# Performance work log

Hardware: AMD Instinct MI355X
Metric: run time of the kernel (lower is better)

The kernel has to match this reference:

```python
import jax, jax.numpy as jnp
import numpy as np

B, L, F = 16, 2048, 512


def setup_inputs() -> dict:
    key = jax.random.key(0)
    k1, k2 = jax.random.split(key)
    feature = jax.random.normal(k1, (B, L, F), dtype=jnp.float32)
    noise = jax.random.normal(k2, (B, L, L), dtype=jnp.float32)
    return {"feature": feature, "noise": noise}


def reference(feature, noise):
    # augmenting_path = softmax over last dim of (B, L, L) gaussian noise
    augmenting_path = jax.nn.softmax(noise, axis=-1)
    # einsum 'bij,bjf->bif': mix frames along the sequence dim
    augmented_feature = jnp.einsum('bij,bjf->bif', augmenting_path, feature)
    return augmented_feature
```

## Files before the change

kernel.cpp:

```cpp
#include <hip/hip_runtime.h>
#include <hip/hip_bf16.h>


#define NB 16
#define SL 2048
#define NF 512
#define TM 128
#define BK 32
#define NT 512
#define NKB (SL / BK)

typedef __bf16 bf16x8 __attribute__((ext_vector_type(8)));
typedef float  f32x4  __attribute__((ext_vector_type(4)));

__device__ __forceinline__ unsigned int f2bf(float x) {
    union { float f; unsigned int u; } v; v.f = x;
    return (v.u + 0x7FFFu + ((v.u >> 16) & 1u)) >> 16;
}

__global__ __launch_bounds__(256, 4)
void feat_panelize(const float* __restrict__ feat, unsigned short* __restrict__ featP) {
    __shared__ unsigned short Lt[32][270];
    const int t  = threadIdx.x;
    const int n0 = blockIdx.x * 256;
    const int kb = blockIdx.y;
    const int b  = blockIdx.z;
    const float* src = feat + ((size_t)b * SL + (size_t)kb * BK) * NF + n0;
    const int j  = t >> 3;
    const int c0 = (t & 7) << 2;
    #pragma unroll
    for (int c = 0; c < 8; ++c) {
        const float4 v = *(const float4*)(src + (size_t)j * NF + c0 + (c << 5));
        unsigned short* p = &Lt[j][c0 + (c << 5)];
        p[0] = (unsigned short)f2bf(v.x); p[1] = (unsigned short)f2bf(v.y);
        p[2] = (unsigned short)f2bf(v.z); p[3] = (unsigned short)f2bf(v.w);
    }
    __syncthreads();
    unsigned int w[16];
    #pragma unroll
    for (int m = 0; m < 16; ++m)
        w[m] = (unsigned int)Lt[2 * m][t] | ((unsigned int)Lt[2 * m + 1][t] << 16);
    unsigned short* dst = featP + ((size_t)(b * NKB + kb) * NF + (size_t)(n0 + t)) * BK;
    #pragma unroll
    for (int c = 0; c < 4; ++c)
        *(uint4*)(dst + (c << 3)) = *(const uint4*)&w[c << 2];
}

__global__ __launch_bounds__(NT, 2)
void frame_augment(const float* __restrict__ noise,
                   const unsigned short* __restrict__ featP,
                   float* __restrict__ out) {
    __shared__ __align__(16) unsigned short As[2][TM][BK];
    __shared__ __align__(16) unsigned short Bs[2][NF][BK];
    __shared__ float part[TM][4];
    __shared__ float linv[TM];

    const int tid  = threadIdx.x;
    const int lane = tid & 63;
    const int wv   = tid >> 6;
    const int n    = blockIdx.x;
    const int b    = ((n & 7) << 1) | ((n >> 3) & 1);
    const int i0   = (n >> 4) * TM;

    const float* noise_b = noise + ((size_t)b * SL + i0) * SL;
    const unsigned short* featB = featP + (size_t)b * NKB * NF * BK;
    float* out_b = out + ((size_t)b * SL + i0) * NF;

    const int ar = tid >> 2;
    const int ac = (tid & 3) << 3;
    const int fm = lane & 15;
    const int fq = lane >> 4;

    f32x4 acc[8][4];
    #pragma unroll
    for (int mi = 0; mi < 8; ++mi)
        #pragma unroll
        for (int ni = 0; ni < 4; ++ni)
            acc[mi][ni] = (f32x4){0.f, 0.f, 0.f, 0.f};

    float rowsum = 0.f;
    const float* a_src = noise_b + (size_t)ar * SL + ac;

    float4 nv0 = *(const float4*)(a_src);
    float4 nv1 = *(const float4*)(a_src + 4);
    {
        const float e0=__expf(nv0.x), e1=__expf(nv0.y), e2=__expf(nv0.z), e3=__expf(nv0.w);
        const float e4=__expf(nv1.x), e5=__expf(nv1.y), e6=__expf(nv1.z), e7=__expf(nv1.w);
        rowsum += ((e0+e1)+(e2+e3)) + ((e4+e5)+(e6+e7));
        uint4 p;
        p.x = f2bf(e0) | (f2bf(e1) << 16);  p.y = f2bf(e2) | (f2bf(e3) << 16);
        p.z = f2bf(e4) | (f2bf(e5) << 16);  p.w = f2bf(e6) | (f2bf(e7) << 16);
        *(uint4*)&As[0][ar][ac] = p;
    }
    {
        const unsigned short* panel = featB;
        #pragma unroll
        for (int c = 0; c < 4; ++c) {
            const int q = (c << 9) + tid;
            __builtin_amdgcn_global_load_lds(
                (const __attribute__((address_space(1))) unsigned int*)(panel + (size_t)q * 8),
                (__attribute__((address_space(3))) unsigned int*)&Bs[0][q >> 2][(q & 3) << 3],
                16, 0, 0);
        }
    }
    nv0 = *(const float4*)(a_src + BK);
    nv1 = *(const float4*)(a_src + BK + 4);
    __syncthreads();

    for (int kb = 0; kb < NKB; ++kb) {
        const int cur = kb & 1, nxt = cur ^ 1;

        if (kb + 1 < NKB) {
            const unsigned short* panel = featB + (size_t)(kb + 1) * NF * BK;
            #pragma unroll
            for (int c = 0; c < 4; ++c) {
                const int q = (c << 9) + tid;
                __builtin_amdgcn_global_load_lds(
                    (const __attribute__((address_space(1))) unsigned int*)(panel + (size_t)q * 8),
                    (__attribute__((address_space(3))) unsigned int*)&Bs[nxt][q >> 2][(q & 3) << 3],
                    16, 0, 0);
            }
            const float e0=__expf(nv0.x), e1=__expf(nv0.y), e2=__expf(nv0.z), e3=__expf(nv0.w);
            const float e4=__expf(nv1.x), e5=__expf(nv1.y), e6=__expf(nv1.z), e7=__expf(nv1.w);
            rowsum += ((e0+e1)+(e2+e3)) + ((e4+e5)+(e6+e7));
            uint4 p;
            p.x = f2bf(e0) | (f2bf(e1) << 16);  p.y = f2bf(e2) | (f2bf(e3) << 16);
            p.z = f2bf(e4) | (f2bf(e5) << 16);  p.w = f2bf(e6) | (f2bf(e7) << 16);
            *(uint4*)&As[nxt][ar][ac] = p;
        }
        if (kb + 2 < NKB) {
            nv0 = *(const float4*)(a_src + (size_t)(kb + 2) * BK);
            nv1 = *(const float4*)(a_src + (size_t)(kb + 2) * BK + 4);
        }

        bf16x8 af[8], bfr[4];
        #pragma unroll
        for (int mi = 0; mi < 8; ++mi)
            af[mi] = *(const bf16x8*)&As[cur][mi * 16 + fm][fq << 3];
        #pragma unroll
        for (int ni = 0; ni < 4; ++ni)
            bfr[ni] = *(const bf16x8*)&Bs[cur][(wv << 6) + ni * 16 + fm][fq << 3];
        #pragma unroll
        for (int mi = 0; mi < 8; ++mi)
            #pragma unroll
            for (int ni = 0; ni < 4; ++ni)
                acc[mi][ni] = __builtin_amdgcn_mfma_f32_16x16x32_bf16(
                    af[mi], bfr[ni], acc[mi][ni], 0, 0, 0);
        __syncthreads();
    }

    part[ar][tid & 3] = rowsum;
    __syncthreads();
    if (tid < TM) {
        const float* q = part[tid];
        linv[tid] = 1.0f / (((q[0] + q[1]) + (q[2] + q[3])));
    }
    __syncthreads();

    #pragma unroll
    for (int mi = 0; mi < 8; ++mi) {
        #pragma unroll
        for (int r = 0; r < 4; ++r) {
            const int row = mi * 16 + (fq << 2) + r;
            const float sc = linv[row];
            float* orow = out_b + (size_t)row * NF + (wv << 6) + fm;
            #pragma unroll
            for (int ni = 0; ni < 4; ++ni)
                orow[ni * 16] = acc[mi][ni][r] * sc;
        }
    }
}

extern "C" void kernel_launch(void* const* d_in, const int* in_sizes, int n_in,
                              void* d_out, int out_size, void* d_ws, size_t ws_size,
                              hipStream_t stream) {
    (void)in_sizes; (void)n_in; (void)out_size; (void)ws_size;
    const float* feat  = (const float*)d_in[0];
    const float* noise = (const float*)d_in[1];
    float* outp = (float*)d_out;
    unsigned short* featP = (unsigned short*)d_ws;

    feat_panelize<<<dim3(NF / 256, NKB, NB), 256, 0, stream>>>(feat, featP);
    frame_augment<<<dim3(SL / TM * NB), NT, 0, stream>>>(noise, featP, outp);
}
```

Before: 461.3 us.

## Read B fragments directly from global, double K tile, pad A in LDS

The feature panel is no longer staged through shared memory. Each wave now loads its B fragments straight from the pre-panelized global buffer into registers. The K tile doubles to 64 and the loop is unrolled by two, which halves the number of barriers, and the exp/softmax staging for the next tile is interleaved between the two MFMA halves. A rows are padded to a stride of 72 to reduce LDS bank conflicts, and removing Bs frees most of the LDS, at the cost of relying on L2/global latency for B with no explicit prefetch.

```diff
diff --git a/kernel.cpp b/kernel.cpp
--- a/kernel.cpp
+++ b/kernel.cpp
@@ -6,9 +6,11 @@
 #define SL 2048
 #define NF 512
 #define TM 128
-#define BK 32
+#define BK 64
+#define NKB (SL / BK)
+#define NPKB (SL / 32)
 #define NT 512
-#define NKB (SL / BK)
+#define ASTRIDE 72
 
 typedef __bf16 bf16x8 __attribute__((ext_vector_type(8)));
 typedef float  f32x4  __attribute__((ext_vector_type(4)));
@@ -25,7 +27,7 @@
     const int n0 = blockIdx.x * 256;
     const int kb = blockIdx.y;
     const int b  = blockIdx.z;
-    const float* src = feat + ((size_t)b * SL + (size_t)kb * BK) * NF + n0;
+    const float* src = feat + ((size_t)b * SL + (size_t)kb * 32) * NF + n0;
     const int j  = t >> 3;
     const int c0 = (t & 7) << 2;
     #pragma unroll
@@ -40,18 +42,71 @@
     #pragma unroll
     for (int m = 0; m < 16; ++m)
         w[m] = (unsigned int)Lt[2 * m][t] | ((unsigned int)Lt[2 * m + 1][t] << 16);
-    unsigned short* dst = featP + ((size_t)(b * NKB + kb) * NF + (size_t)(n0 + t)) * BK;
+    unsigned short* dst = featP + ((size_t)(b * NPKB + kb) * NF + (size_t)(n0 + t)) * 32;
     #pragma unroll
     for (int c = 0; c < 4; ++c)
         *(uint4*)(dst + (c << 3)) = *(const uint4*)&w[c << 2];
 }
+
+
+#define FA_BODY(KB, CUR, CONS, LOADB)                                          \
+    {                                                                          \
+        const int kb_ = (KB);                                                  \
+        const int nxt_ = (CUR) ^ 1;                                            \
+        if (kb_ + 2 < NKB) {                                                   \
+            const float* np_ = a_src + (size_t)(kb_ + 2) * BK;                 \
+            _Pragma("unroll")                                                  \
+            for (int c = 0; c < 4; ++c) LOADB[c] = *(const float4*)(np_ + (c << 2)); \
+        }                                                                      \
+        const unsigned short* pan_ = featB + (size_t)(kb_ << 1) * (NF * 32);   \
+        bf16x8 bfr0[4], bfr1[4];                                               \
+        _Pragma("unroll")                                                      \
+        for (int ni = 0; ni < 4; ++ni)                                         \
+            bfr0[ni] = *(const bf16x8*)(pan_ + (size_t)(((wv << 6) + (ni << 4) + fm) << 5) + (fq << 3)); \
+        _Pragma("unroll")                                                      \
+        for (int ni = 0; ni < 4; ++ni)                                         \
+            bfr1[ni] = *(const bf16x8*)(pan_ + NF * 32 + (size_t)(((wv << 6) + (ni << 4) + fm) << 5) + (fq << 3)); \
+        _Pragma("unroll")                                                      \
+        for (int mi = 0; mi < 8; ++mi) {                                       \
+            const bf16x8 af_ = *(const bf16x8*)&As[CUR][(mi << 4) + fm][fq << 3]; \
+            _Pragma("unroll")                                                  \
+            for (int ni = 0; ni < 4; ++ni)                                     \
+                acc[mi][ni] = __builtin_amdgcn_mfma_f32_16x16x32_bf16(af_, bfr0[ni], acc[mi][ni], 0, 0, 0); \
+        }                                                                      \
+        if (kb_ + 1 < NKB) {                                                   \
+            const float e0_ = __expf(CONS[0].x), e1_ = __expf(CONS[0].y);      \
+            const float e2_ = __expf(CONS[0].z), e3_ = __expf(CONS[0].w);      \
+            const float e4_ = __expf(CONS[1].x), e5_ = __expf(CONS[1].y);      \
+            const float e6_ = __expf(CONS[1].z), e7_ = __expf(CONS[1].w);      \
+            const float e8_ = __expf(CONS[2].x), e9_ = __expf(CONS[2].y);      \
+            const float ea_ = __expf(CONS[2].z), eb_ = __expf(CONS[2].w);      \
+            const float ec_ = __expf(CONS[3].x), ed_ = __expf(CONS[3].y);      \
+            const float ee_ = __expf(CONS[3].z), ef_ = __expf(CONS[3].w);      \
+            rowsum += (((e0_+e1_)+(e2_+e3_)) + ((e4_+e5_)+(e6_+e7_)))          \
+                    + (((e8_+e9_)+(ea_+eb_)) + ((ec_+ed_)+(ee_+ef_)));         \
+            uint4 q0_, q1_;                                                    \
+            q0_.x = f2bf(e0_) | (f2bf(e1_) << 16); q0_.y = f2bf(e2_) | (f2bf(e3_) << 16); \
+            q0_.z = f2bf(e4_) | (f2bf(e5_) << 16); q0_.w = f2bf(e6_) | (f2bf(e7_) << 16); \
+            q1_.x = f2bf(e8_) | (f2bf(e9_) << 16); q1_.y = f2bf(ea_) | (f2bf(eb_) << 16); \
+            q1_.z = f2bf(ec_) | (f2bf(ed_) << 16); q1_.w = f2bf(ee_) | (f2bf(ef_) << 16); \
+            *(uint4*)&As[nxt_][ar][ac] = q0_;                                  \
+            *(uint4*)&As[nxt_][ar][ac + 8] = q1_;                              \
+        }                                                                      \
+        _Pragma("unroll")                                                      \
+        for (int mi = 0; mi < 8; ++mi) {                                       \
+            const bf16x8 af_ = *(const bf16x8*)&As[CUR][(mi << 4) + fm][32 + (fq << 3)]; \
+            _Pragma("unroll")                                                  \
+            for (int ni = 0; ni < 4; ++ni)                                     \
+                acc[mi][ni] = __builtin_amdgcn_mfma_f32_16x16x32_bf16(af_, bfr1[ni], acc[mi][ni], 0, 0, 0); \
+        }                                                                      \
+        __syncthreads();                                                       \
+    }
 
 __global__ __launch_bounds__(NT, 2)
 void frame_augment(const float* __restrict__ noise,
                    const unsigned short* __restrict__ featP,
                    float* __restrict__ out) {
-    __shared__ __align__(16) unsigned short As[2][TM][BK];
-    __shared__ __align__(16) unsigned short Bs[2][NF][BK];
+    __shared__ __align__(16) unsigned short As[2][TM][ASTRIDE];
     __shared__ float part[TM][4];
     __shared__ float linv[TM];
 
@@ -63,11 +118,11 @@
     const int i0   = (n >> 4) * TM;
 
     const float* noise_b = noise + ((size_t)b * SL + i0) * SL;
-    const unsigned short* featB = featP + (size_t)b * NKB * NF * BK;
+    const unsigned short* featB = featP + (size_t)b * NPKB * NF * 32;
     float* out_b = out + ((size_t)b * SL + i0) * NF;
 
     const int ar = tid >> 2;
-    const int ac = (tid & 3) << 3;
+    const int ac = (tid & 3) << 4;
     const int fm = lane & 15;
     const int fq = lane >> 4;
 
@@ -81,79 +136,42 @@
     float rowsum = 0.f;
     const float* a_src = noise_b + (size_t)ar * SL + ac;
 
-    float4 nv0 = *(const float4*)(a_src);
-    float4 nv1 = *(const float4*)(a_src + 4);
+    float4 nvA[4], nvB[4];
+    #pragma unroll
+    for (int c = 0; c < 4; ++c) nvB[c] = *(const float4*)(a_src + (c << 2));
     {
-        const float e0=__expf(nv0.x), e1=__expf(nv0.y), e2=__expf(nv0.z), e3=__expf(nv0.w);
-        const float e4=__expf(nv1.x), e5=__expf(nv1.y), e6=__expf(nv1.z), e7=__expf(nv1.w);
-        rowsum += ((e0+e1)+(e2+e3)) + ((e4+e5)+(e6+e7));
-        uint4 p;
-        p.x = f2bf(e0) | (f2bf(e1) << 16);  p.y = f2bf(e2) | (f2bf(e3) << 16);
-        p.z = f2bf(e4) | (f2bf(e5) << 16);  p.w = f2bf(e6) | (f2bf(e7) << 16);
-        *(uint4*)&As[0][ar][ac] = p;
-    }
-    {
-        const unsigned short* panel = featB;
-        #pragma unroll
-        for (int c = 0; c < 4; ++c) {
-            const int q = (c << 9) + tid;
-            __builtin_amdgcn_global_load_lds(
-                (const __attribute__((address_space(1))) unsigned int*)(panel + (size_t)q * 8),
-                (__attribute__((address_space(3))) unsigned int*)&Bs[0][q >> 2][(q & 3) << 3],
-                16, 0, 0);
-        }
-    }
-    nv0 = *(const float4*)(a_src + BK);
-    nv1 = *(const float4*)(a_src + BK + 4);
-    __syncthreads();
-
-    for (int kb = 0; kb < NKB; ++kb) {
-        const int cur = kb & 1, nxt = cur ^ 1;
-
-        if (kb + 1 < NKB) {
-            const unsigned short* panel = featB + (size_t)(kb + 1) * NF * BK;
-            #pragma unroll
-            for (int c = 0; c < 4; ++c) {
-                const int q = (c << 9) + tid;
-                __builtin_amdgcn_global_load_lds(
-                    (const __attribute__((address_space(1))) unsigned int*)(panel + (size_t)q * 8),
-                    (__attribute__((address_space(3))) unsigned int*)&Bs[nxt][q >> 2][(q & 3) << 3],
-                    16, 0, 0);
-            }
-            const float e0=__expf(nv0.x), e1=__expf(nv0.y), e2=__expf(nv0.z), e3=__expf(nv0.w);
-            const float e4=__expf(nv1.x), e5=__expf(nv1.y), e6=__expf(nv1.z), e7=__expf(nv1.w);
-            rowsum += ((e0+e1)+(e2+e3)) + ((e4+e5)+(e6+e7));
-            uint4 p;
-            p.x = f2bf(e0) | (f2bf(e1) << 16);  p.y = f2bf(e2) | (f2bf(e3) << 16);
-            p.z = f2bf(e4) | (f2bf(e5) << 16);  p.w = f2bf(e6) | (f2bf(e7) << 16);
-            *(uint4*)&As[nxt][ar][ac] = p;
-        }
-        if (kb + 2 < NKB) {
-            nv0 = *(const float4*)(a_src + (size_t)(kb + 2) * BK);
-            nv1 = *(const float4*)(a_src + (size_t)(kb + 2) * BK + 4);
-        }
-
-        bf16x8 af[8], bfr[4];
-        #pragma unroll
-        for (int mi = 0; mi < 8; ++mi)
-            af[mi] = *(const bf16x8*)&As[cur][mi * 16 + fm][fq << 3];
-        #pragma unroll
-        for (int ni = 0; ni < 4; ++ni)
-            bfr[ni] = *(const bf16x8*)&Bs[cur][(wv << 6) + ni * 16 + fm][fq << 3];
-        #pragma unroll
-        for (int mi = 0; mi < 8; ++mi)
-            #pragma unroll
-            for (int ni = 0; ni < 4; ++ni)
-                acc[mi][ni] = __builtin_amdgcn_mfma_f32_16x16x32_bf16(
-                    af[mi], bfr[ni], acc[mi][ni], 0, 0, 0);
-        __syncthreads();
+        const float e0 = __expf(nvB[0].x), e1 = __expf(nvB[0].y);
+        const float e2 = __expf(nvB[0].z), e3 = __expf(nvB[0].w);
+        const float e4 = __expf(nvB[1].x), e5 = __expf(nvB[1].y);
+        const float e6 = __expf(nvB[1].z), e7 = __expf(nvB[1].w);
+        const float e8 = __expf(nvB[2].x), e9 = __expf(nvB[2].y);
+        const float ea = __expf(nvB[2].z), eb = __expf(nvB[2].w);
+        const float ec = __expf(nvB[3].x), ed = __expf(nvB[3].y);
+        const float ee = __expf(nvB[3].z), ef = __expf(nvB[3].w);
+        rowsum += (((e0+e1)+(e2+e3)) + ((e4+e5)+(e6+e7)))
+                + (((e8+e9)+(ea+eb)) + ((ec+ed)+(ee+ef)));
+        uint4 q0, q1;
+        q0.x = f2bf(e0) | (f2bf(e1) << 16); q0.y = f2bf(e2) | (f2bf(e3) << 16);
+        q0.z = f2bf(e4) | (f2bf(e5) << 16); q0.w = f2bf(e6) | (f2bf(e7) << 16);
+        q1.x = f2bf(e8) | (f2bf(e9) << 16); q1.y = f2bf(ea) | (f2bf(eb) << 16);
+        q1.z = f2bf(ec) | (f2bf(ed) << 16); q1.w = f2bf(ee) | (f2bf(ef) << 16);
+        *(uint4*)&As[0][ar][ac] = q0;
+        *(uint4*)&As[0][ar][ac + 8] = q1;
+    }
+    #pragma unroll
+    for (int c = 0; c < 4; ++c) nvA[c] = *(const float4*)(a_src + BK + (c << 2));
+    __syncthreads();
+
+    for (int kbp = 0; kbp < NKB; kbp += 2) {
+        FA_BODY(kbp,     0, nvA, nvB)
+        FA_BODY(kbp + 1, 1, nvB, nvA)
     }
 
     part[ar][tid & 3] = rowsum;
     __syncthreads();
     if (tid < TM) {
         const float* q = part[tid];
-        linv[tid] = 1.0f / (((q[0] + q[1]) + (q[2] + q[3])));
+        linv[tid] = 1.0f / ((q[0] + q[1]) + (q[2] + q[3]));
     }
     __syncthreads();
 
@@ -180,6 +198,6 @@
     float* outp = (float*)d_out;
     unsigned short* featP = (unsigned short*)d_ws;
 
-    feat_panelize<<<dim3(NF / 256, NKB, NB), 256, 0, stream>>>(feat, featP);
+    feat_panelize<<<dim3(NF / 256, NPKB, NB), 256, 0, stream>>>(feat, featP);
     frame_augment<<<dim3(SL / TM * NB), NT, 0, stream>>>(noise, featP, outp);
 }
```

Result: slower. 589.5 us (+27.8%).
